# Optimization experiments

Hardware: AMD Instinct MI355X
Metric: run time of the kernel (lower is better)

## Reference

```python
import jax, jax.numpy as jnp
import numpy as np

L, B, E, H = 1024, 8, 512, 8
D = E // H
THRESH = 0.1  # sparsity_threshold
W_STD = 0.1   # keeps logits spread so threshold mask is non-trivial


def setup_inputs() -> dict:
    k0 = jax.random.key(0)
    ks = jax.random.split(k0, 7)
    return {
        "query": jax.random.normal(ks[0], (L, B, E), jnp.float32),
        "key": jax.random.normal(ks[1], (L, B, E), jnp.float32),
        "value": jax.random.normal(ks[2], (L, B, E), jnp.float32),
        "Wq": jax.random.normal(ks[3], (E, E), jnp.float32) * W_STD,
        "bq": jnp.zeros((E,), jnp.float32),
        "Wk": jax.random.normal(ks[4], (E, E), jnp.float32) * W_STD,
        "bk": jnp.zeros((E,), jnp.float32),
    }


def reference(query, key, value, Wq, bq, Wk, bk):
    # query/key/value: (L, B, E), seq-first as in nn.MultiheadAttention
    Lq, Bq, Eq = query.shape
    S = key.shape[0]
    q = (query @ Wq.T + bq).reshape(Lq, Bq, H, D)
    k = (key @ Wk.T + bk).reshape(S, Bq, H, D)
    scale = 1.0 / jnp.sqrt(jnp.asarray(D, q.dtype))
    scores = jnp.einsum('lbhd,sbhd->bhls', q, k) * scale  # [B,H,L,S]
    attn = jax.nn.softmax(scores, axis=-1)
    attn_avg = attn.mean(axis=1)  # averaged over heads -> [B,L,S]
    # threshold-mask + renormalize
    sw = jnp.where(attn_avg > THRESH, attn_avg, jnp.zeros((), attn_avg.dtype))
    sw = sw / (sw.sum(axis=-1, keepdims=True) + 1e-6)
    # second matmul against the RAW value tensor: [B,L,S] @ [B,S,E] -> [L,B,E]
    out = jnp.einsum('bls,sbe->lbe', sw, value)
    return out, sw
```

## Files before the change

kernel.cpp:

```cpp
#include <hip/hip_runtime.h>


#define THRESH 0.1f
#define PLANE (8 * 8 * 1024 * 64)

typedef __attribute__((ext_vector_type(8))) short bf8_t;
typedef __attribute__((ext_vector_type(4))) float f4_t;

#define MFMA16(a, b, c) __builtin_amdgcn_mfma_f32_16x16x32_bf16(a, b, c, 0, 0, 0)

__device__ __forceinline__ unsigned short f2bf(float x) {
  unsigned int u = __float_as_uint(x);
  u += 0x7FFFu + ((u >> 16) & 1u);
  return (unsigned short)(u >> 16);
}
__device__ __forceinline__ float bf2f(unsigned short h) {
  return __uint_as_float(((unsigned int)h) << 16);
}

__global__ __launch_bounds__(256) void proj_kernel(
    const float* __restrict__ A,
    const float* __restrict__ W,
    const float* __restrict__ bias,
    unsigned short* __restrict__ outp)
{
  __shared__ float As[16][132];
  __shared__ float Ws[16][132];
  const int t  = threadIdx.x;
  const int bm = blockIdx.x;
  const int bn = blockIdx.y;
  const int ty = t >> 4;
  const int tx = t & 15;
  const int lr  = t >> 2;
  const int lc4 = (t & 3) << 2;

  const float* Arow0 = A + (size_t)(bm * 128 + lr) * 512 + lc4;
  const float* Arow1 = Arow0 + 64 * 512;
  const float* Wrow0 = W + (size_t)(bn * 128 + lr) * 512 + lc4;
  const float* Wrow1 = Wrow0 + 64 * 512;

  float acc[8][8] = {};

  for (int k0 = 0; k0 < 512; k0 += 16) {
    float4 a0 = *(const float4*)(Arow0 + k0);
    float4 a1 = *(const float4*)(Arow1 + k0);
    float4 w0 = *(const float4*)(Wrow0 + k0);
    float4 w1 = *(const float4*)(Wrow1 + k0);
    __syncthreads();
    As[lc4 + 0][lr] = a0.x; As[lc4 + 1][lr] = a0.y; As[lc4 + 2][lr] = a0.z; As[lc4 + 3][lr] = a0.w;
    As[lc4 + 0][lr + 64] = a1.x; As[lc4 + 1][lr + 64] = a1.y; As[lc4 + 2][lr + 64] = a1.z; As[lc4 + 3][lr + 64] = a1.w;
    Ws[lc4 + 0][lr] = w0.x; Ws[lc4 + 1][lr] = w0.y; Ws[lc4 + 2][lr] = w0.z; Ws[lc4 + 3][lr] = w0.w;
    Ws[lc4 + 0][lr + 64] = w1.x; Ws[lc4 + 1][lr + 64] = w1.y; Ws[lc4 + 2][lr + 64] = w1.z; Ws[lc4 + 3][lr + 64] = w1.w;
    __syncthreads();
    #pragma unroll
    for (int kk = 0; kk < 16; ++kk) {
      float4 av0 = *(const float4*)&As[kk][ty * 8];
      float4 av1 = *(const float4*)&As[kk][ty * 8 + 4];
      float4 bv0 = *(const float4*)&Ws[kk][tx * 8];
      float4 bv1 = *(const float4*)&Ws[kk][tx * 8 + 4];
      float ar[8] = {av0.x, av0.y, av0.z, av0.w, av1.x, av1.y, av1.z, av1.w};
      float br[8] = {bv0.x, bv0.y, bv0.z, bv0.w, bv1.x, bv1.y, bv1.z, bv1.w};
      #pragma unroll
      for (int i = 0; i < 8; ++i)
        #pragma unroll
        for (int j = 0; j < 8; ++j)
          acc[i][j] += ar[i] * br[j];
    }
  }

  #pragma unroll
  for (int i = 0; i < 8; ++i) {
    const int gr = bm * 128 + ty * 8 + i;
    const int l = gr >> 3;
    const int b = gr & 7;
    #pragma unroll
    for (int jv = 0; jv < 8; jv += 4) {
      const int gc = bn * 128 + tx * 8 + jv;
      const int h = gc >> 6;
      const int d = gc & 63;
      const size_t off = ((size_t)((b * 8 + h) * 1024 + l)) * 64 + d;
      ushort4 ph, pm, pl;
      #pragma unroll
      for (int q = 0; q < 4; ++q) {
        float x = acc[i][jv + q] + bias[gc + q];
        unsigned short b1 = f2bf(x);  float r1 = x  - bf2f(b1);
        unsigned short b2 = f2bf(r1); float r2 = r1 - bf2f(b2);
        unsigned short b3 = f2bf(r2);
        ((unsigned short*)&ph)[q] = b1;
        ((unsigned short*)&pm)[q] = b2;
        ((unsigned short*)&pl)[q] = b3;
      }
      *(ushort4*)&outp[off] = ph;
      *(ushort4*)&outp[(size_t)PLANE + off] = pm;
      *(ushort4*)&outp[(size_t)2 * PLANE + off] = pl;
    }
  }
}

__global__ __launch_bounds__(512, 2) void attn_mfma_kernel(
    const unsigned short* __restrict__ qs,
    const unsigned short* __restrict__ ks,
    float* __restrict__ sw)
{
  const int bx = blockIdx.x;
  const int b  = bx & 7;
  const int l0 = (bx >> 3) << 5;
  const int tid  = threadIdx.x;
  const int w    = tid >> 6;
  const int lane = tid & 63;
  const int c    = lane & 15;
  const int g    = lane >> 4;

  __shared__ float red[8][32];
  __shared__ float redc[32];

  f4_t avg[2][8];
  #pragma unroll
  for (int rt = 0; rt < 2; ++rt)
    #pragma unroll
    for (int ct = 0; ct < 8; ++ct)
      avg[rt][ct] = (f4_t){0.f, 0.f, 0.f, 0.f};

  for (int h = 0; h < 8; ++h) {
    const size_t qbase = ((size_t)((b * 8 + h) * 1024 + l0)) * 64;
    const size_t kbase = ((size_t)((b * 8 + h) * 1024)) * 64;

    bf8_t qf[3][2][2];
    #pragma unroll
    for (int p = 0; p < 3; ++p)
      #pragma unroll
      for (int rt = 0; rt < 2; ++rt)
        #pragma unroll
        for (int kc = 0; kc < 2; ++kc)
          qf[p][rt][kc] = *(const bf8_t*)&qs[(size_t)p * PLANE + qbase +
                                             (size_t)(rt * 16 + c) * 64 + kc * 32 + g * 8];

    f4_t acc[2][8];
    #pragma unroll
    for (int rt = 0; rt < 2; ++rt)
      #pragma unroll
      for (int ct = 0; ct < 8; ++ct)
        acc[rt][ct] = (f4_t){0.f, 0.f, 0.f, 0.f};

    #pragma unroll
    for (int ct = 0; ct < 8; ++ct) {
      const size_t kb = kbase + (size_t)(w * 128 + ct * 16 + c) * 64 + g * 8;
      #pragma unroll
      for (int kc = 0; kc < 2; ++kc) {
        bf8_t kh = *(const bf8_t*)&ks[kb + kc * 32];
        bf8_t km = *(const bf8_t*)&ks[(size_t)PLANE + kb + kc * 32];
        bf8_t kl = *(const bf8_t*)&ks[(size_t)2 * PLANE + kb + kc * 32];
        #pragma unroll
        for (int rt = 0; rt < 2; ++rt) {
          acc[rt][ct] = MFMA16(qf[0][rt][kc], kh, acc[rt][ct]);
          acc[rt][ct] = MFMA16(qf[0][rt][kc], km, acc[rt][ct]);
          acc[rt][ct] = MFMA16(qf[1][rt][kc], kh, acc[rt][ct]);
          acc[rt][ct] = MFMA16(qf[0][rt][kc], kl, acc[rt][ct]);
          acc[rt][ct] = MFMA16(qf[1][rt][kc], km, acc[rt][ct]);
          acc[rt][ct] = MFMA16(qf[2][rt][kc], kh, acc[rt][ct]);
        }
      }
    }

    float mloc[2][4];
    #pragma unroll
    for (int rt = 0; rt < 2; ++rt)
      #pragma unroll
      for (int reg = 0; reg < 4; ++reg) {
        float m = acc[rt][0][reg];
        #pragma unroll
        for (int ct = 1; ct < 8; ++ct) m = fmaxf(m, acc[rt][ct][reg]);
        #pragma unroll
        for (int off = 8; off > 0; off >>= 1) m = fmaxf(m, __shfl_xor(m, off));
        mloc[rt][reg] = m;
      }
    if (c == 0) {
      #pragma unroll
      for (int rt = 0; rt < 2; ++rt)
        #pragma unroll
        for (int reg = 0; reg < 4; ++reg)
          red[w][rt * 16 + g * 4 + reg] = mloc[rt][reg];
    }
    __syncthreads();
    if (tid < 32) {
      float m = red[0][tid];
      #pragma unroll
      for (int w2 = 1; w2 < 8; ++w2) m = fmaxf(m, red[w2][tid]);
      redc[tid] = m;
    }
    __syncthreads();
    float mrow[2][4];
    #pragma unroll
    for (int rt = 0; rt < 2; ++rt)
      #pragma unroll
      for (int reg = 0; reg < 4; ++reg)
        mrow[rt][reg] = redc[rt * 16 + g * 4 + reg];

    float sloc[2][4] = {};
    #pragma unroll
    for (int rt = 0; rt < 2; ++rt)
      #pragma unroll
      for (int ct = 0; ct < 8; ++ct)
        #pragma unroll
        for (int reg = 0; reg < 4; ++reg) {
          float p = __expf(0.125f * (acc[rt][ct][reg] - mrow[rt][reg]));
          acc[rt][ct][reg] = p;
          sloc[rt][reg] += p;
        }
    #pragma unroll
    for (int rt = 0; rt < 2; ++rt)
      #pragma unroll
      for (int reg = 0; reg < 4; ++reg) {
        float s = sloc[rt][reg];
        #pragma unroll
        for (int off = 8; off > 0; off >>= 1) s += __shfl_xor(s, off);
        sloc[rt][reg] = s;
      }
    if (c == 0) {
      #pragma unroll
      for (int rt = 0; rt < 2; ++rt)
        #pragma unroll
        for (int reg = 0; reg < 4; ++reg)
          red[w][rt * 16 + g * 4 + reg] = sloc[rt][reg];
    }
    __syncthreads();
    if (tid < 32) {
      float s = red[0][tid];
      #pragma unroll
      for (int w2 = 1; w2 < 8; ++w2) s += red[w2][tid];
      redc[tid] = s;
    }
    __syncthreads();
    #pragma unroll
    for (int rt = 0; rt < 2; ++rt)
      #pragma unroll
      for (int reg = 0; reg < 4; ++reg) {
        const float inv = 0.125f / redc[rt * 16 + g * 4 + reg];
        #pragma unroll
        for (int ct = 0; ct < 8; ++ct)
          avg[rt][ct][reg] += acc[rt][ct][reg] * inv;
      }
  }

  float tl[2][4] = {};
  #pragma unroll
  for (int rt = 0; rt < 2; ++rt)
    #pragma unroll
    for (int ct = 0; ct < 8; ++ct)
      #pragma unroll
      for (int reg = 0; reg < 4; ++reg) {
        float v = avg[rt][ct][reg];
        v = v > THRESH ? v : 0.f;
        avg[rt][ct][reg] = v;
        tl[rt][reg] += v;
      }
  #pragma unroll
  for (int rt = 0; rt < 2; ++rt)
    #pragma unroll
    for (int reg = 0; reg < 4; ++reg) {
      float s = tl[rt][reg];
      #pragma unroll
      for (int off = 8; off > 0; off >>= 1) s += __shfl_xor(s, off);
      tl[rt][reg] = s;
    }
  if (c == 0) {
    #pragma unroll
    for (int rt = 0; rt < 2; ++rt)
      #pragma unroll
      for (int reg = 0; reg < 4; ++reg)
        red[w][rt * 16 + g * 4 + reg] = tl[rt][reg];
  }
  __syncthreads();
  if (tid < 32) {
    float s = red[0][tid];
    #pragma unroll
    for (int w2 = 1; w2 < 8; ++w2) s += red[w2][tid];
    redc[tid] = s;
  }
  __syncthreads();
  #pragma unroll
  for (int rt = 0; rt < 2; ++rt)
    #pragma unroll
    for (int reg = 0; reg < 4; ++reg) {
      const float inv = 1.f / (redc[rt * 16 + g * 4 + reg] + 1e-6f);
      const size_t rowoff = ((size_t)(b * 1024 + l0 + rt * 16 + g * 4 + reg)) * 1024;
      #pragma unroll
      for (int ct = 0; ct < 8; ++ct)
        sw[rowoff + w * 128 + ct * 16 + c] = avg[rt][ct][reg] * inv;
    }
}

__global__ __launch_bounds__(128) void pv_kernel(
    const float* __restrict__ sw,
    const float* __restrict__ value,
    float* __restrict__ out)
{
  const int l = blockIdx.x;
  const int b = blockIdx.y;
  const int t = threadIdx.x;
  __shared__ int cnt;
  __shared__ int   sidx[32];
  __shared__ float swt[32];
  if (t == 0) cnt = 0;
  __syncthreads();

  const float* row = sw + (size_t)(b * 1024 + l) * 1024;
  #pragma unroll
  for (int it = 0; it < 2; ++it) {
    const int s0 = (t + it * 128) * 4;
    float4 v = *(const float4*)(row + s0);
    if (v.x > 0.f) { int i = atomicAdd(&cnt, 1); if (i < 32) { sidx[i] = s0 + 0; swt[i] = v.x; } }
    if (v.y > 0.f) { int i = atomicAdd(&cnt, 1); if (i < 32) { sidx[i] = s0 + 1; swt[i] = v.y; } }
    if (v.z > 0.f) { int i = atomicAdd(&cnt, 1); if (i < 32) { sidx[i] = s0 + 2; swt[i] = v.z; } }
    if (v.w > 0.f) { int i = atomicAdd(&cnt, 1); if (i < 32) { sidx[i] = s0 + 3; swt[i] = v.w; } }
  }
  __syncthreads();
  const int n = cnt < 32 ? cnt : 32;

  const int e0 = t * 4;
  float4 o = {0.f, 0.f, 0.f, 0.f};
  for (int j = 0; j < n; ++j) {
    const float wgt = swt[j];
    const float4 vv = *(const float4*)(value + (size_t)(sidx[j] * 8 + b) * 512 + e0);
    o.x += wgt * vv.x; o.y += wgt * vv.y; o.z += wgt * vv.z; o.w += wgt * vv.w;
  }
  *(float4*)&out[(size_t)(l * 8 + b) * 512 + e0] = o;
}

extern "C" void kernel_launch(void* const* d_in, const int* in_sizes, int n_in,
                              void* d_out, int out_size, void* d_ws, size_t ws_size,
                              hipStream_t stream) {
  const float* query = (const float*)d_in[0];
  const float* key   = (const float*)d_in[1];
  const float* value = (const float*)d_in[2];
  const float* Wq    = (const float*)d_in[3];
  const float* bq    = (const float*)d_in[4];
  const float* Wk    = (const float*)d_in[5];
  const float* bk    = (const float*)d_in[6];

  float* out = (float*)d_out;
  float* sw  = out + (size_t)1024 * 8 * 512;

  unsigned short* qs = (unsigned short*)d_ws;
  unsigned short* ks = qs + (size_t)3 * PLANE;

  proj_kernel<<<dim3(64, 4), 256, 0, stream>>>(query, Wq, bq, qs);
  proj_kernel<<<dim3(64, 4), 256, 0, stream>>>(key,   Wk, bk, ks);
  attn_mfma_kernel<<<256, 512, 0, stream>>>(qs, ks, sw);
  pv_kernel<<<dim3(1024, 8), 128, 0, stream>>>(sw, value, out);
}
```

Before: 388.6 us.

## Merge Q/K projections, prefetch loads, and double-buffer reductions in attention kernel

The two projection launches are merged into one grid using a z dimension, and each block's N tile shrinks to 64 columns, so twice as many blocks run. The projection's global loads are register-prefetched one k-step ahead. The attention kernel double-buffers K fragments and prefetches the next head's Q and K while the current head computes. Its reductions now use parity-indexed shared buffers with a single raw barrier per reduction, where there were two __syncthreads before. Launch bounds drop to one block per CU minimum, which allows more registers at the risk of lower occupancy.

```diff
diff --git a/kernel.cpp b/kernel.cpp
--- a/kernel.cpp
+++ b/kernel.cpp
@@ -19,13 +19,19 @@
 }
 
 __global__ __launch_bounds__(256) void proj_kernel(
-    const float* __restrict__ A,
-    const float* __restrict__ W,
-    const float* __restrict__ bias,
-    unsigned short* __restrict__ outp)
+    const float* __restrict__ query, const float* __restrict__ key,
+    const float* __restrict__ Wq,    const float* __restrict__ Wk,
+    const float* __restrict__ bq,    const float* __restrict__ bk,
+    unsigned short* __restrict__ outq, unsigned short* __restrict__ outk)
 {
+  const int z = blockIdx.z;
+  const float* A    = z ? key : query;
+  const float* W    = z ? Wk  : Wq;
+  const float* bias = z ? bk  : bq;
+  unsigned short* outp = z ? outk : outq;
+
   __shared__ float As[16][132];
-  __shared__ float Ws[16][132];
+  __shared__ float Ws[16][68];
   const int t  = threadIdx.x;
   const int bm = blockIdx.x;
   const int bn = blockIdx.y;
@@ -36,68 +42,66 @@
 
   const float* Arow0 = A + (size_t)(bm * 128 + lr) * 512 + lc4;
   const float* Arow1 = Arow0 + 64 * 512;
-  const float* Wrow0 = W + (size_t)(bn * 128 + lr) * 512 + lc4;
-  const float* Wrow1 = Wrow0 + 64 * 512;
-
-  float acc[8][8] = {};
+  const float* Wrow  = W + (size_t)(bn * 64 + lr) * 512 + lc4;
+
+  float acc[8][4] = {};
+
+  float4 a0 = *(const float4*)(Arow0);
+  float4 a1 = *(const float4*)(Arow1);
+  float4 w0 = *(const float4*)(Wrow);
 
   for (int k0 = 0; k0 < 512; k0 += 16) {
-    float4 a0 = *(const float4*)(Arow0 + k0);
-    float4 a1 = *(const float4*)(Arow1 + k0);
-    float4 w0 = *(const float4*)(Wrow0 + k0);
-    float4 w1 = *(const float4*)(Wrow1 + k0);
     __syncthreads();
     As[lc4 + 0][lr] = a0.x; As[lc4 + 1][lr] = a0.y; As[lc4 + 2][lr] = a0.z; As[lc4 + 3][lr] = a0.w;
     As[lc4 + 0][lr + 64] = a1.x; As[lc4 + 1][lr + 64] = a1.y; As[lc4 + 2][lr + 64] = a1.z; As[lc4 + 3][lr + 64] = a1.w;
     Ws[lc4 + 0][lr] = w0.x; Ws[lc4 + 1][lr] = w0.y; Ws[lc4 + 2][lr] = w0.z; Ws[lc4 + 3][lr] = w0.w;
-    Ws[lc4 + 0][lr + 64] = w1.x; Ws[lc4 + 1][lr + 64] = w1.y; Ws[lc4 + 2][lr + 64] = w1.z; Ws[lc4 + 3][lr + 64] = w1.w;
     __syncthreads();
+    if (k0 + 16 < 512) {
+      a0 = *(const float4*)(Arow0 + k0 + 16);
+      a1 = *(const float4*)(Arow1 + k0 + 16);
+      w0 = *(const float4*)(Wrow  + k0 + 16);
+    }
     #pragma unroll
     for (int kk = 0; kk < 16; ++kk) {
       float4 av0 = *(const float4*)&As[kk][ty * 8];
       float4 av1 = *(const float4*)&As[kk][ty * 8 + 4];
-      float4 bv0 = *(const float4*)&Ws[kk][tx * 8];
-      float4 bv1 = *(const float4*)&Ws[kk][tx * 8 + 4];
+      float4 bv0 = *(const float4*)&Ws[kk][tx * 4];
       float ar[8] = {av0.x, av0.y, av0.z, av0.w, av1.x, av1.y, av1.z, av1.w};
-      float br[8] = {bv0.x, bv0.y, bv0.z, bv0.w, bv1.x, bv1.y, bv1.z, bv1.w};
+      float br[4] = {bv0.x, bv0.y, bv0.z, bv0.w};
       #pragma unroll
       for (int i = 0; i < 8; ++i)
         #pragma unroll
-        for (int j = 0; j < 8; ++j)
+        for (int j = 0; j < 4; ++j)
           acc[i][j] += ar[i] * br[j];
     }
   }
 
+  const int h = bn;
   #pragma unroll
   for (int i = 0; i < 8; ++i) {
     const int gr = bm * 128 + ty * 8 + i;
     const int l = gr >> 3;
     const int b = gr & 7;
-    #pragma unroll
-    for (int jv = 0; jv < 8; jv += 4) {
-      const int gc = bn * 128 + tx * 8 + jv;
-      const int h = gc >> 6;
-      const int d = gc & 63;
-      const size_t off = ((size_t)((b * 8 + h) * 1024 + l)) * 64 + d;
-      ushort4 ph, pm, pl;
-      #pragma unroll
-      for (int q = 0; q < 4; ++q) {
-        float x = acc[i][jv + q] + bias[gc + q];
-        unsigned short b1 = f2bf(x);  float r1 = x  - bf2f(b1);
-        unsigned short b2 = f2bf(r1); float r2 = r1 - bf2f(b2);
-        unsigned short b3 = f2bf(r2);
-        ((unsigned short*)&ph)[q] = b1;
-        ((unsigned short*)&pm)[q] = b2;
-        ((unsigned short*)&pl)[q] = b3;
-      }
-      *(ushort4*)&outp[off] = ph;
-      *(ushort4*)&outp[(size_t)PLANE + off] = pm;
-      *(ushort4*)&outp[(size_t)2 * PLANE + off] = pl;
-    }
-  }
-}
-
-__global__ __launch_bounds__(512, 2) void attn_mfma_kernel(
+    const int d = tx * 4;
+    const size_t off = ((size_t)((b * 8 + h) * 1024 + l)) * 64 + d;
+    ushort4 ph, pm, pl;
+    #pragma unroll
+    for (int q = 0; q < 4; ++q) {
+      float x = acc[i][q] + bias[h * 64 + d + q];
+      unsigned short b1 = f2bf(x);  float r1 = x  - bf2f(b1);
+      unsigned short b2 = f2bf(r1); float r2 = r1 - bf2f(b2);
+      unsigned short b3 = f2bf(r2);
+      ((unsigned short*)&ph)[q] = b1;
+      ((unsigned short*)&pm)[q] = b2;
+      ((unsigned short*)&pl)[q] = b3;
+    }
+    *(ushort4*)&outp[off] = ph;
+    *(ushort4*)&outp[(size_t)PLANE + off] = pm;
+    *(ushort4*)&outp[(size_t)2 * PLANE + off] = pl;
+  }
+}
+
+__global__ __launch_bounds__(512, 1) void attn_mfma_kernel(
     const unsigned short* __restrict__ qs,
     const unsigned short* __restrict__ ks,
     float* __restrict__ sw)
@@ -111,8 +115,15 @@
   const int c    = lane & 15;
   const int g    = lane >> 4;
 
-  __shared__ float red[8][32];
-  __shared__ float redc[32];
+  __shared__ float mred[2][8][32];
+  __shared__ float sred[2][8][32];
+
+#define KADDR(H, CT, KC, PL) \
+  ((const bf8_t*)&ks[(size_t)(PL) * PLANE + \
+      ((size_t)((b * 8 + (H)) * 1024 + w * 128 + (CT) * 16 + c)) * 64 + (KC) * 32 + g * 8])
+#define QADDR(H, RT, KC, PL) \
+  ((const bf8_t*)&qs[(size_t)(PL) * PLANE + \
+      ((size_t)((b * 8 + (H)) * 1024 + l0 + (RT) * 16 + c)) * 64 + (KC) * 32 + g * 8])
 
   f4_t avg[2][8];
   #pragma unroll
@@ -121,19 +132,22 @@
     for (int ct = 0; ct < 8; ++ct)
       avg[rt][ct] = (f4_t){0.f, 0.f, 0.f, 0.f};
 
+  bf8_t kb[2][3];
+  bf8_t qf[3][2][2];
+
+  #pragma unroll
+  for (int pl = 0; pl < 3; ++pl) {
+    kb[0][pl] = *KADDR(0, 0, 0, pl);
+    kb[1][pl] = *KADDR(0, 0, 1, pl);
+    #pragma unroll
+    for (int rt = 0; rt < 2; ++rt)
+      #pragma unroll
+      for (int kc = 0; kc < 2; ++kc)
+        qf[pl][rt][kc] = *QADDR(0, rt, kc, pl);
+  }
+
   for (int h = 0; h < 8; ++h) {
-    const size_t qbase = ((size_t)((b * 8 + h) * 1024 + l0)) * 64;
-    const size_t kbase = ((size_t)((b * 8 + h) * 1024)) * 64;
-
-    bf8_t qf[3][2][2];
-    #pragma unroll
-    for (int p = 0; p < 3; ++p)
-      #pragma unroll
-      for (int rt = 0; rt < 2; ++rt)
-        #pragma unroll
-        for (int kc = 0; kc < 2; ++kc)
-          qf[p][rt][kc] = *(const bf8_t*)&qs[(size_t)p * PLANE + qbase +
-                                             (size_t)(rt * 16 + c) * 64 + kc * 32 + g * 8];
+    const int par = h & 1;
 
     f4_t acc[2][8];
     #pragma unroll
@@ -143,26 +157,39 @@
         acc[rt][ct] = (f4_t){0.f, 0.f, 0.f, 0.f};
 
     #pragma unroll
-    for (int ct = 0; ct < 8; ++ct) {
-      const size_t kb = kbase + (size_t)(w * 128 + ct * 16 + c) * 64 + g * 8;
-      #pragma unroll
-      for (int kc = 0; kc < 2; ++kc) {
-        bf8_t kh = *(const bf8_t*)&ks[kb + kc * 32];
-        bf8_t km = *(const bf8_t*)&ks[(size_t)PLANE + kb + kc * 32];
-        bf8_t kl = *(const bf8_t*)&ks[(size_t)2 * PLANE + kb + kc * 32];
-        #pragma unroll
-        for (int rt = 0; rt < 2; ++rt) {
-          acc[rt][ct] = MFMA16(qf[0][rt][kc], kh, acc[rt][ct]);
-          acc[rt][ct] = MFMA16(qf[0][rt][kc], km, acc[rt][ct]);
-          acc[rt][ct] = MFMA16(qf[1][rt][kc], kh, acc[rt][ct]);
-          acc[rt][ct] = MFMA16(qf[0][rt][kc], kl, acc[rt][ct]);
-          acc[rt][ct] = MFMA16(qf[1][rt][kc], km, acc[rt][ct]);
-          acc[rt][ct] = MFMA16(qf[2][rt][kc], kh, acc[rt][ct]);
-        }
-      }
-    }
-
-    float mloc[2][4];
+    for (int u = 0; u < 16; ++u) {
+      const int ct = u >> 1, kc = u & 1, p = u & 1;
+      const bf8_t kh = kb[p][0], km = kb[p][1], kl = kb[p][2];
+      #pragma unroll
+      for (int rt = 0; rt < 2; ++rt) {
+        acc[rt][ct] = MFMA16(qf[0][rt][kc], kh, acc[rt][ct]);
+        acc[rt][ct] = MFMA16(qf[0][rt][kc], km, acc[rt][ct]);
+        acc[rt][ct] = MFMA16(qf[1][rt][kc], kh, acc[rt][ct]);
+        acc[rt][ct] = MFMA16(qf[0][rt][kc], kl, acc[rt][ct]);
+        acc[rt][ct] = MFMA16(qf[1][rt][kc], km, acc[rt][ct]);
+        acc[rt][ct] = MFMA16(qf[2][rt][kc], kh, acc[rt][ct]);
+      }
+      if (u + 2 < 16) {
+        #pragma unroll
+        for (int pl = 0; pl < 3; ++pl)
+          kb[p][pl] = *KADDR(h, (u + 2) >> 1, (u + 2) & 1, pl);
+      } else if (h < 7) {
+        #pragma unroll
+        for (int pl = 0; pl < 3; ++pl)
+          kb[p][pl] = *KADDR(h + 1, (u - 14) >> 1, u & 1, pl);
+      }
+    }
+
+    if (h < 7) {
+      #pragma unroll
+      for (int pl = 0; pl < 3; ++pl)
+        #pragma unroll
+        for (int rt = 0; rt < 2; ++rt)
+          #pragma unroll
+          for (int kc = 0; kc < 2; ++kc)
+            qf[pl][rt][kc] = *QADDR(h + 1, rt, kc, pl);
+    }
+
     #pragma unroll
     for (int rt = 0; rt < 2; ++rt)
       #pragma unroll
@@ -172,29 +199,21 @@
         for (int ct = 1; ct < 8; ++ct) m = fmaxf(m, acc[rt][ct][reg]);
         #pragma unroll
         for (int off = 8; off > 0; off >>= 1) m = fmaxf(m, __shfl_xor(m, off));
-        mloc[rt][reg] = m;
-      }
-    if (c == 0) {
-      #pragma unroll
-      for (int rt = 0; rt < 2; ++rt)
-        #pragma unroll
-        for (int reg = 0; reg < 4; ++reg)
-          red[w][rt * 16 + g * 4 + reg] = mloc[rt][reg];
-    }
-    __syncthreads();
-    if (tid < 32) {
-      float m = red[0][tid];
-      #pragma unroll
-      for (int w2 = 1; w2 < 8; ++w2) m = fmaxf(m, red[w2][tid]);
-      redc[tid] = m;
-    }
-    __syncthreads();
+        if (c == 0) mred[par][w][rt * 16 + g * 4 + reg] = m;
+      }
+    asm volatile("s_waitcnt lgkmcnt(0)\n\ts_barrier" ::: "memory");
     float mrow[2][4];
     #pragma unroll
-    for (int rt = 0; rt < 2; ++rt)
-      #pragma unroll
-      for (int reg = 0; reg < 4; ++reg)
-        mrow[rt][reg] = redc[rt * 16 + g * 4 + reg];
+    for (int rt = 0; rt < 2; ++rt) {
+      float4 m4 = *(const float4*)&mred[par][0][rt * 16 + g * 4];
+      #pragma unroll
+      for (int w2 = 1; w2 < 8; ++w2) {
+        float4 v = *(const float4*)&mred[par][w2][rt * 16 + g * 4];
+        m4.x = fmaxf(m4.x, v.x); m4.y = fmaxf(m4.y, v.y);
+        m4.z = fmaxf(m4.z, v.z); m4.w = fmaxf(m4.w, v.w);
+      }
+      mrow[rt][0] = m4.x; mrow[rt][1] = m4.y; mrow[rt][2] = m4.z; mrow[rt][3] = m4.w;
+    }
 
     float sloc[2][4] = {};
     #pragma unroll
@@ -214,32 +233,26 @@
         float s = sloc[rt][reg];
         #pragma unroll
         for (int off = 8; off > 0; off >>= 1) s += __shfl_xor(s, off);
-        sloc[rt][reg] = s;
-      }
-    if (c == 0) {
-      #pragma unroll
-      for (int rt = 0; rt < 2; ++rt)
-        #pragma unroll
-        for (int reg = 0; reg < 4; ++reg)
-          red[w][rt * 16 + g * 4 + reg] = sloc[rt][reg];
-    }
-    __syncthreads();
-    if (tid < 32) {
-      float s = red[0][tid];
-      #pragma unroll
-      for (int w2 = 1; w2 < 8; ++w2) s += red[w2][tid];
-      redc[tid] = s;
-    }
-    __syncthreads();
-    #pragma unroll
-    for (int rt = 0; rt < 2; ++rt)
+        if (c == 0) sred[par][w][rt * 16 + g * 4 + reg] = s;
+      }
+    asm volatile("s_waitcnt lgkmcnt(0)\n\ts_barrier" ::: "memory");
+    #pragma unroll
+    for (int rt = 0; rt < 2; ++rt) {
+      float4 s4 = *(const float4*)&sred[par][0][rt * 16 + g * 4];
+      #pragma unroll
+      for (int w2 = 1; w2 < 8; ++w2) {
+        float4 v = *(const float4*)&sred[par][w2][rt * 16 + g * 4];
+        s4.x += v.x; s4.y += v.y; s4.z += v.z; s4.w += v.w;
+      }
+      float ssum[4] = {s4.x, s4.y, s4.z, s4.w};
       #pragma unroll
       for (int reg = 0; reg < 4; ++reg) {
-        const float inv = 0.125f / redc[rt * 16 + g * 4 + reg];
+        const float inv = 0.125f / ssum[reg];
         #pragma unroll
         for (int ct = 0; ct < 8; ++ct)
           avg[rt][ct][reg] += acc[rt][ct][reg] * inv;
       }
+    }
   }
 
   float tl[2][4] = {};
@@ -261,33 +274,29 @@
       float s = tl[rt][reg];
       #pragma unroll
       for (int off = 8; off > 0; off >>= 1) s += __shfl_xor(s, off);
-      tl[rt][reg] = s;
-    }
-  if (c == 0) {
-    #pragma unroll
-    for (int rt = 0; rt < 2; ++rt)
-      #pragma unroll
-      for (int reg = 0; reg < 4; ++reg)
-        red[w][rt * 16 + g * 4 + reg] = tl[rt][reg];
-  }
+      if (c == 0) mred[0][w][rt * 16 + g * 4 + reg] = s;
+    }
   __syncthreads();
-  if (tid < 32) {
-    float s = red[0][tid];
-    #pragma unroll
-    for (int w2 = 1; w2 < 8; ++w2) s += red[w2][tid];
-    redc[tid] = s;
-  }
-  __syncthreads();
-  #pragma unroll
-  for (int rt = 0; rt < 2; ++rt)
+  #pragma unroll
+  for (int rt = 0; rt < 2; ++rt) {
+    float4 s4 = *(const float4*)&mred[0][0][rt * 16 + g * 4];
+    #pragma unroll
+    for (int w2 = 1; w2 < 8; ++w2) {
+      float4 v = *(const float4*)&mred[0][w2][rt * 16 + g * 4];
+      s4.x += v.x; s4.y += v.y; s4.z += v.z; s4.w += v.w;
+    }
+    float ts[4] = {s4.x, s4.y, s4.z, s4.w};
     #pragma unroll
     for (int reg = 0; reg < 4; ++reg) {
-      const float inv = 1.f / (redc[rt * 16 + g * 4 + reg] + 1e-6f);
+      const float inv = 1.f / (ts[reg] + 1e-6f);
       const size_t rowoff = ((size_t)(b * 1024 + l0 + rt * 16 + g * 4 + reg)) * 1024;
       #pragma unroll
       for (int ct = 0; ct < 8; ++ct)
         sw[rowoff + w * 128 + ct * 16 + c] = avg[rt][ct][reg] * inv;
     }
+  }
+#undef KADDR
+#undef QADDR
 }
 
 __global__ __launch_bounds__(128) void pv_kernel(
@@ -344,8 +353,7 @@
   unsigned short* qs = (unsigned short*)d_ws;
   unsigned short* ks = qs + (size_t)3 * PLANE;
 
-  proj_kernel<<<dim3(64, 4), 256, 0, stream>>>(query, Wq, bq, qs);
-  proj_kernel<<<dim3(64, 4), 256, 0, stream>>>(key,   Wk, bk, ks);
+  proj_kernel<<<dim3(64, 8, 2), 256, 0, stream>>>(query, key, Wq, Wk, bq, bk, qs, ks);
   attn_mfma_kernel<<<256, 512, 0, stream>>>(qs, ks, sw);
   pv_kernel<<<dim3(1024, 8), 128, 0, stream>>>(sw, value, out);
 }
```

Result: no change. 381.7 us (-1.8%).
